# Kernel optimization log

Measured on AMD Instinct MI355X. Metric: run time of the kernel, lower is better.

Reference implementation:

```python
import math
import jax, jax.numpy as jnp
import numpy as np

D = 512
H = 8
HD = D // H
FF = 2048
EPS = 1e-5


def _layernorm(x, gamma, beta):
    mean = jnp.mean(x, axis=-1, keepdims=True)
    var = jnp.mean((x - mean) ** 2, axis=-1, keepdims=True)
    return gamma * (x - mean) / jnp.sqrt(var + EPS) + beta


def _attention(q, k, v, mask):
    # q,k,v: [B,H,Sq/Sk,hd]; mask: [B,Sq,Sk] additive, broadcast over heads
    scale = 1.0 / math.sqrt(q.shape[-1])
    scores = jnp.einsum('bhqd,bhkd->bhqk', q, k) * scale
    scores = scores + mask[:, None, :, :]
    probs = jax.nn.softmax(scores, axis=-1)
    return jnp.einsum('bhqk,bhkd->bhqd', probs, v)


def setup_inputs() -> dict:
    key = jax.random.key(0)
    ks = jax.random.split(key, 20)
    B, S_ENC, S_DEC = 256, 512, 64
    s = 0.02
    inp = {
        'x': jax.random.normal(ks[0], (B, S_ENC, D), jnp.float32),
        'y': jax.random.normal(ks[1], (B, S_DEC, D), jnp.float32),
        'mask': jnp.zeros((B, S_DEC, S_DEC), jnp.float32),
        'mask2': jnp.zeros((B, S_DEC, S_ENC), jnp.float32),
        # self-attention params
        'qkv_w': jax.random.normal(ks[2], (D, 3 * D), jnp.float32) * s,
        'qkv_b': jnp.zeros((3 * D,), jnp.float32),
        'sa_out_w': jax.random.normal(ks[3], (D, D), jnp.float32) * s,
        'sa_out_b': jnp.zeros((D,), jnp.float32),
        # cross-attention params
        'q_w': jax.random.normal(ks[4], (D, D), jnp.float32) * s,
        'q_b': jnp.zeros((D,), jnp.float32),
        'kv_w': jax.random.normal(ks[5], (D, 2 * D), jnp.float32) * s,
        'kv_b': jnp.zeros((2 * D,), jnp.float32),
        'ca_out_w': jax.random.normal(ks[6], (D, D), jnp.float32) * s,
        'ca_out_b': jnp.zeros((D,), jnp.float32),
        # ffn params
        'l1_w': jax.random.normal(ks[7], (D, FF), jnp.float32) * s,
        'l1_b': jnp.zeros((FF,), jnp.float32),
        'l2_w': jax.random.normal(ks[8], (FF, D), jnp.float32) * s,
        'l2_b': jnp.zeros((D,), jnp.float32),
        # layernorm params
        'g1': jnp.ones((D,), jnp.float32), 'b1': jnp.zeros((D,), jnp.float32),
        'g2': jnp.ones((D,), jnp.float32), 'b2': jnp.zeros((D,), jnp.float32),
        'g3': jnp.ones((D,), jnp.float32), 'b3': jnp.zeros((D,), jnp.float32),
    }
    return inp


def reference(x, y, mask, mask2, qkv_w, qkv_b, sa_out_w, sa_out_b,
              q_w, q_b, kv_w, kv_b, ca_out_w, ca_out_b,
              l1_w, l1_b, l2_w, l2_b, g1, b1, g2, b2, g3, b3):
    B, Sd, _ = y.shape
    Se = x.shape[1]

    # --- self attention (post-norm, dropout is identity at eval) ---
    resid = y
    qkv = y @ qkv_w + qkv_b                     # [B,Sd,3D]
    qkv = qkv.reshape(B, Sd, H, 3 * HD).transpose(0, 2, 1, 3)
    q, k, v = jnp.split(qkv, 3, axis=-1)        # each [B,H,Sd,hd]
    vals = _attention(q, k, v, mask)
    vals = vals.transpose(0, 2, 1, 3).reshape(B, Sd, D)
    y = vals @ sa_out_w + sa_out_b
    y = _layernorm(y + resid, g1, b1)

    # --- cross attention: kv from encoder x, q from decoder y ---
    resid = y
    kv = x @ kv_w + kv_b                        # [B,Se,2D]
    kv = kv.reshape(B, Se, H, 2 * HD).transpose(0, 2, 1, 3)
    k, v = jnp.split(kv, 2, axis=-1)            # each [B,H,Se,hd]
    q = (y @ q_w + q_b).reshape(B, Sd, H, HD).transpose(0, 2, 1, 3)
    vals = _attention(q, k, v, mask2)
    vals = vals.transpose(0, 2, 1, 3).reshape(B, Sd, D)
    y = vals @ ca_out_w + ca_out_b
    y = _layernorm(y + resid, g2, b2)

    # --- feed forward ---
    resid = y
    h = jax.nn.relu(y @ l1_w + l1_b)
    y = h @ l2_w + l2_b
    y = _layernorm(y + resid, g3, b3)
    return y
```

## Files before the change

### kernel.cpp

```cpp
#include <hip/hip_runtime.h>
#include <hip/hip_bf16.h>
#include <stdint.h>


#define SDEC 64
#define SENC 512
#define DMODEL 512
#define FFDIM 2048

typedef __bf16 bf16x8 __attribute__((ext_vector_type(8)));
typedef float  f32x4  __attribute__((ext_vector_type(4)));

static __device__ __forceinline__ float bf2f(unsigned short u) {
  union { unsigned int i; float f; } w; w.i = ((unsigned int)u) << 16; return w.f;
}
static __device__ __forceinline__ unsigned short f2bf(float f) {
  union { float f; unsigned int i; } w; w.f = f;
  unsigned int u = w.i;
  return (unsigned short)((u + 0x7fffu + ((u >> 16) & 1u)) >> 16);
}

static __device__ __forceinline__ void gl_lds16(const unsigned short* g, unsigned short* l) {
  __builtin_amdgcn_global_load_lds(
      (const __attribute__((address_space(1))) unsigned int*)g,
      (__attribute__((address_space(3))) unsigned int*)l,
      16, 0, 0);
}

__global__ __launch_bounds__(256)
void cvt_f32_bf16(const float* __restrict__ in, unsigned short* __restrict__ out, size_t n8)
{
  size_t i = (size_t)blockIdx.x * blockDim.x + threadIdx.x;
  const size_t stride = (size_t)gridDim.x * blockDim.x;
  for (; i < n8; i += stride) {
    const float* p = in + i * 8;
    float4 a = *(const float4*)p, b = *(const float4*)(p + 4);
    union { unsigned short s[8]; uint4 v; } u;
    u.s[0] = f2bf(a.x); u.s[1] = f2bf(a.y); u.s[2] = f2bf(a.z); u.s[3] = f2bf(a.w);
    u.s[4] = f2bf(b.x); u.s[5] = f2bf(b.y); u.s[6] = f2bf(b.z); u.s[7] = f2bf(b.w);
    *(uint4*)(out + i * 8) = u.v;
  }
}

#define GEMM_COMPUTE(asrc, bsrc)                                                     \
  {                                                                                  \
    const unsigned short* as_ = (asrc);                                              \
    const unsigned short* bs_ = (bsrc);                                              \
    bf16x8 af[4], bfr[4];                                                            \
    _Pragma("unroll")                                                                \
    for (int mi = 0; mi < 4; ++mi)                                                   \
      af[mi] = *(const bf16x8*)&as_[(wm * 64 + mi * 16 + fr) * 32 + fk];             \
    _Pragma("unroll")                                                                \
    for (int ni = 0; ni < 4; ++ni)                                                   \
      bfr[ni] = *(const bf16x8*)&bs_[(wn * 64 + ni * 16 + fr) * 32 + fk];            \
    _Pragma("unroll")                                                                \
    for (int mi = 0; mi < 4; ++mi)                                                   \
      _Pragma("unroll")                                                              \
      for (int ni = 0; ni < 4; ++ni)                                                 \
        acc[mi][ni] = __builtin_amdgcn_mfma_f32_16x16x32_bf16(af[mi], bfr[ni],       \
                                                              acc[mi][ni], 0, 0, 0); \
  }

template<int RELU>
__global__ __launch_bounds__(256, 2)
void gemm_kernel(const unsigned short* __restrict__ A, const unsigned short* __restrict__ Bt,
                 const float* __restrict__ bias, unsigned short* __restrict__ C,
                 int M, int N, int K)
{
  __shared__ unsigned short sh[2 * 8192];
  const int tid = threadIdx.x;

  const int gx   = gridDim.x;
  const int nwg  = gx * gridDim.y;
  const int orig = blockIdx.y * gx + blockIdx.x;
  const int wg   = (orig & 7) * (nwg >> 3) + (orig >> 3);
  const int row0 = (wg / gx) * 128;
  const int col0 = (wg % gx) * 128;

  const int w = tid >> 6, lane = tid & 63;
  const int wm = w >> 1, wn = w & 1;
  const int gr = lane >> 2, gc = (lane & 3) * 8;

  auto STAGE = [&](int k0, int buf) {
    unsigned short* as = sh + buf * 8192;
    unsigned short* bs = as + 4096;
    #pragma unroll
    for (int i = 0; i < 2; ++i) {
      const int rbase = w * 32 + i * 16;
      gl_lds16(A  + (size_t)(row0 + rbase + gr) * K + (k0 + gc), as + rbase * 32);
      gl_lds16(Bt + (size_t)(col0 + rbase + gr) * K + (k0 + gc), bs + rbase * 32);
    }
  };

  f32x4 acc[4][4];
  #pragma unroll
  for (int i = 0; i < 4; ++i)
    #pragma unroll
    for (int j = 0; j < 4; ++j)
      acc[i][j] = (f32x4){0.f, 0.f, 0.f, 0.f};

  const int fr = lane & 15, fk = (lane >> 4) * 8;

  STAGE(0, 0);
  int cur = 0;
  for (int k0 = 0; k0 + 32 < K; k0 += 32) {
    STAGE(k0 + 32, cur ^ 1);
    asm volatile("s_waitcnt vmcnt(4)" ::: "memory");
    __builtin_amdgcn_s_barrier();
    asm volatile("" ::: "memory");
    GEMM_COMPUTE(sh + cur * 8192, sh + cur * 8192 + 4096);
    asm volatile("" ::: "memory");
    __builtin_amdgcn_s_barrier();
    cur ^= 1;
  }
  asm volatile("s_waitcnt vmcnt(0)" ::: "memory");
  __builtin_amdgcn_s_barrier();
  asm volatile("" ::: "memory");
  GEMM_COMPUTE(sh + cur * 8192, sh + cur * 8192 + 4096);
  asm volatile("" ::: "memory");
  __builtin_amdgcn_s_barrier();

  {
    const int fq = lane >> 4;
    #pragma unroll
    for (int ni = 0; ni < 4; ++ni) {
      const int c = wn * 64 + ni * 16 + fr;
      const float bv = bias ? bias[col0 + c] : 0.f;
      #pragma unroll
      for (int mi = 0; mi < 4; ++mi) {
        #pragma unroll
        for (int t = 0; t < 4; ++t) {
          const int r = wm * 64 + mi * 16 + fq * 4 + t;
          float v = acc[mi][ni][t] + bv;
          if (RELU) v = fmaxf(v, 0.f);
          sh[r * 128 + (c ^ (fq << 4))] = f2bf(v);
        }
      }
    }
    __syncthreads();
    const int rr = tid >> 4;
    const int cc = (tid & 15) * 8;
    #pragma unroll
    for (int p = 0; p < 8; ++p) {
      const int r = p * 16 + rr;
      *(uint4*)(C + (size_t)(row0 + r) * N + col0 + cc) =
          *(const uint4*)&sh[r * 128 + (cc ^ (w << 4))];
    }
  }
}

template<int RELU>
__global__ __launch_bounds__(512, 1)
void gemm256_kernel(const unsigned short* __restrict__ A, const unsigned short* __restrict__ Bt,
                    const float* __restrict__ bias, unsigned short* __restrict__ C,
                    int M, int N, int K)
{
  __shared__ unsigned short sh[65536];
  const int tid = threadIdx.x;

  const int gx   = gridDim.x;
  const int nwg  = gx * gridDim.y;
  const int orig = blockIdx.y * gx + blockIdx.x;
  const int wg   = (orig & 7) * (nwg >> 3) + (orig >> 3);
  const int row0 = (wg / gx) * 256;
  const int col0 = (wg % gx) * 256;

  const int w = tid >> 6, lane = tid & 63;
  const int wm = w >> 2, wn = w & 3;
  const int fr = lane & 15, fg = lane >> 4;

  const int srl = lane >> 3;
  const int sgc = ((lane & 7) ^ srl) * 8;

  auto STAGE_PART = [&](int k0, int buf, int part) {
    unsigned short* base = sh + buf * 32768 + ((part >= 2) ? 16384 : 0);
    const unsigned short* G = (part >= 2) ? Bt : A;
    const int o0 = (part >= 2) ? col0 : row0;
    const int ph = part & 1;
    #pragma unroll
    for (int j = 0; j < 2; ++j) {
      const int rt = w * 32 + ph * 16 + j * 8;
      gl_lds16(G + (size_t)(o0 + rt + srl) * K + (k0 + sgc), base + rt * 64);
    }
  };

  f32x4 acc[8][4];
  #pragma unroll
  for (int i = 0; i < 8; ++i)
    #pragma unroll
    for (int j = 0; j < 4; ++j)
      acc[i][j] = (f32x4){0.f, 0.f, 0.f, 0.f};

  const int NT = K >> 6;
  #pragma unroll
  for (int part = 0; part < 4; ++part) STAGE_PART(0, 0, part);

  for (int t = 0; t < NT; ++t) {
    const int buf = t & 1;
    const unsigned short* as = sh + buf * 32768;
    const unsigned short* bs = as + 16384;
    const int kn = (t + 1) << 6;
    asm volatile("s_waitcnt vmcnt(0)" ::: "memory");
    __builtin_amdgcn_sched_barrier(0);
    __builtin_amdgcn_s_barrier();

    #pragma unroll
    for (int ks = 0; ks < 2; ++ks) {
      #pragma unroll
      for (int mh = 0; mh < 2; ++mh) {
        bf16x8 af[4], bfv[4];
        #pragma unroll
        for (int i = 0; i < 4; ++i) {
          const int row = wm * 128 + (mh * 4 + i) * 16 + fr;
          af[i] = *(const bf16x8*)&as[row * 64 + (((ks * 4 + fg) ^ (fr & 7)) * 8)];
        }
        #pragma unroll
        for (int i = 0; i < 4; ++i) {
          const int row = wn * 64 + i * 16 + fr;
          bfv[i] = *(const bf16x8*)&bs[row * 64 + (((ks * 4 + fg) ^ (fr & 7)) * 8)];
        }
        if (t + 1 < NT) {
          const int ph = ks * 2 + mh;
          if (ph == 0) { STAGE_PART(kn, buf ^ 1, 0); STAGE_PART(kn, buf ^ 1, 1); }
          if (ph == 1) { STAGE_PART(kn, buf ^ 1, 2); STAGE_PART(kn, buf ^ 1, 3); }
        }
        asm volatile("" ::: "memory");
        __builtin_amdgcn_s_barrier();
        __builtin_amdgcn_s_setprio(1);
        #pragma unroll
        for (int i = 0; i < 4; ++i)
          #pragma unroll
          for (int j = 0; j < 4; ++j)
            acc[mh * 4 + i][j] = __builtin_amdgcn_mfma_f32_16x16x32_bf16(
                af[i], bfv[j], acc[mh * 4 + i][j], 0, 0, 0);
        __builtin_amdgcn_s_setprio(0);
        asm volatile("" ::: "memory");
        __builtin_amdgcn_s_barrier();
      }
    }
  }

  {
    #pragma unroll
    for (int j = 0; j < 4; ++j) {
      const int c = wn * 64 + j * 16 + fr;
      const float bv = bias ? bias[col0 + c] : 0.f;
      const int cp = c ^ (fg << 4);
      #pragma unroll
      for (int i = 0; i < 8; ++i) {
        #pragma unroll
        for (int tt = 0; tt < 4; ++tt) {
          const int r = wm * 128 + i * 16 + fg * 4 + tt;
          float v = acc[i][j][tt] + bv;
          if (RELU) v = fmaxf(v, 0.f);
          sh[r * 256 + cp] = f2bf(v);
        }
      }
    }
    __syncthreads();
    const int rr = tid >> 5;
    const int cc = (tid & 31) * 8;
    #pragma unroll
    for (int p = 0; p < 16; ++p) {
      const int r = p * 16 + rr;
      const int rc = (r >> 2) & 3;
      *(uint4*)(C + (size_t)(row0 + r) * N + col0 + cc) =
          *(const uint4*)&sh[r * 256 + (cc ^ (rc << 4))];
    }
  }
}

__global__ __launch_bounds__(256, 2)
void attn_mfma(const unsigned short* __restrict__ qbuf, int qstride, int qmul,
               const unsigned short* __restrict__ kvbuf, int kvstride, int kmul, int kadd,
               int tokmul, int Skv, const float* __restrict__ mask,
               unsigned short* __restrict__ vals, float scale)
{
  __shared__ unsigned short Qs[64 * 72];
  __shared__ unsigned short Ks[64 * 72];
  __shared__ unsigned short Vt[64 * 72];
  __shared__ unsigned short Ps[64 * 72];

  const int nwg  = gridDim.x * gridDim.y;
  const int orig = blockIdx.y * gridDim.x + blockIdx.x;
  const int wg   = (orig & 7) * (nwg >> 3) + (orig >> 3);
  const int h = wg & 7, b = wg >> 3;

  const int tid = threadIdx.x;
  const int w = tid >> 6, lane = tid & 63;
  const int srow = tid >> 2;
  const int sc0 = (tid & 3) * 16;

  {
    const unsigned short* qg = qbuf + (size_t)(b * 64 + srow) * qstride + h * qmul + sc0;
    *(uint4*)&Qs[srow * 72 + sc0]     = *(const uint4*)qg;
    *(uint4*)&Qs[srow * 72 + sc0 + 8] = *(const uint4*)(qg + 8);
  }

  const int fr = lane & 15;
  const int fg = lane >> 4;
  const int orow = fg * 4;

  float mstate[4], lstate[4];
  f32x4 oacc[4];
  #pragma unroll
  for (int t = 0; t < 4; ++t) { mstate[t] = -1e30f; lstate[t] = 0.f; }
  #pragma unroll
  for (int ni = 0; ni < 4; ++ni) oacc[ni] = (f32x4){0.f, 0.f, 0.f, 0.f};

  for (int j0 = 0; j0 < Skv; j0 += 64) {
    __syncthreads();
    {
      const unsigned short* kg = kvbuf + (size_t)(b * tokmul + j0 + srow) * kvstride
                                 + h * kmul + kadd + sc0;
      *(uint4*)&Ks[srow * 72 + sc0]     = *(const uint4*)kg;
      *(uint4*)&Ks[srow * 72 + sc0 + 8] = *(const uint4*)(kg + 8);
      const unsigned short* vg = kg + 64;
      uint4 v0 = *(const uint4*)vg;
      uint4 v1 = *(const uint4*)(vg + 8);
      const unsigned short* vsp = (const unsigned short*)&v0;
      #pragma unroll
      for (int jj = 0; jj < 8; ++jj) Vt[(sc0 + jj) * 72 + srow] = vsp[jj];
      vsp = (const unsigned short*)&v1;
      #pragma unroll
      for (int jj = 0; jj < 8; ++jj) Vt[(sc0 + 8 + jj) * 72 + srow] = vsp[jj];
    }
    __syncthreads();

    f32x4 s[4];
    #pragma unroll
    for (int ni = 0; ni < 4; ++ni) s[ni] = (f32x4){0.f, 0.f, 0.f, 0.f};
    #pragma unroll
    for (int ks = 0; ks < 2; ++ks) {
      bf16x8 aq = *(const bf16x8*)&Qs[(w * 16 + fr) * 72 + ks * 32 + fg * 8];
      #pragma unroll
      for (int ni = 0; ni < 4; ++ni) {
        bf16x8 bk = *(const bf16x8*)&Ks[(ni * 16 + fr) * 72 + ks * 32 + fg * 8];
        s[ni] = __builtin_amdgcn_mfma_f32_16x16x32_bf16(aq, bk, s[ni], 0, 0, 0);
      }
    }

    #pragma unroll
    for (int t = 0; t < 4; ++t) {
      const int grow = w * 16 + orow + t;
      const float* mrow = mask + ((size_t)b * 64 + grow) * Skv + j0;
      float sv[4];
      float tmax = -1e30f;
      #pragma unroll
      for (int ni = 0; ni < 4; ++ni) {
        sv[ni] = s[ni][t] * scale + mrow[ni * 16 + fr];
        tmax = fmaxf(tmax, sv[ni]);
      }
      #pragma unroll
      for (int off = 1; off < 16; off <<= 1) tmax = fmaxf(tmax, __shfl_xor(tmax, off));
      const float mn = fmaxf(mstate[t], tmax);
      const float fscl = __expf(mstate[t] - mn);
      mstate[t] = mn;
      float psum = 0.f;
      #pragma unroll
      for (int ni = 0; ni < 4; ++ni) {
        float p = __expf(sv[ni] - mn);
        psum += p;
        Ps[grow * 72 + ni * 16 + fr] = f2bf(p);
      }
      #pragma unroll
      for (int off = 1; off < 16; off <<= 1) psum += __shfl_xor(psum, off);
      lstate[t] = lstate[t] * fscl + psum;
      #pragma unroll
      for (int ni = 0; ni < 4; ++ni) oacc[ni][t] *= fscl;
    }
    __syncthreads();

    #pragma unroll
    for (int ks = 0; ks < 2; ++ks) {
      bf16x8 pa = *(const bf16x8*)&Ps[(w * 16 + fr) * 72 + ks * 32 + fg * 8];
      #pragma unroll
      for (int ni = 0; ni < 4; ++ni) {
        bf16x8 vb = *(const bf16x8*)&Vt[(ni * 16 + fr) * 72 + ks * 32 + fg * 8];
        oacc[ni] = __builtin_amdgcn_mfma_f32_16x16x32_bf16(pa, vb, oacc[ni], 0, 0, 0);
      }
    }
  }

  #pragma unroll
  for (int t = 0; t < 4; ++t) {
    const int grow = w * 16 + orow + t;
    const float inv = 1.f / lstate[t];
    unsigned short* og = vals + (size_t)(b * 64 + grow) * DMODEL + h * 64;
    #pragma unroll
    for (int ni = 0; ni < 4; ++ni)
      og[ni * 16 + fr] = f2bf(oacc[ni][t] * inv);
  }
}

__global__ __launch_bounds__(256)
void ln_kernel(const unsigned short* __restrict__ proj16, const float* __restrict__ resid32,
               const unsigned short* __restrict__ resid16,
               const float* __restrict__ gamma, const float* __restrict__ beta,
               unsigned short* __restrict__ out16, float* __restrict__ out32)
{
  const int w = threadIdx.x >> 6, lane = threadIdx.x & 63;
  const size_t r = (size_t)blockIdx.x * 4 + w;
  const int d0 = lane * 8;

  float x[8];
  {
    uint4 u = *(const uint4*)(proj16 + r * DMODEL + d0);
    const unsigned short* s = (const unsigned short*)&u;
    #pragma unroll
    for (int j = 0; j < 8; ++j) x[j] = bf2f(s[j]);
  }
  if (resid32) {
    const float* p = resid32 + r * DMODEL + d0;
    float4 a = *(const float4*)p, b = *(const float4*)(p + 4);
    x[0] += a.x; x[1] += a.y; x[2] += a.z; x[3] += a.w;
    x[4] += b.x; x[5] += b.y; x[6] += b.z; x[7] += b.w;
  } else {
    uint4 u = *(const uint4*)(resid16 + r * DMODEL + d0);
    const unsigned short* s = (const unsigned short*)&u;
    #pragma unroll
    for (int j = 0; j < 8; ++j) x[j] += bf2f(s[j]);
  }

  float sum = 0.f;
  #pragma unroll
  for (int j = 0; j < 8; ++j) sum += x[j];
  #pragma unroll
  for (int off = 32; off > 0; off >>= 1) sum += __shfl_xor(sum, off);
  const float mean = sum * (1.f / DMODEL);

  float vs = 0.f;
  #pragma unroll
  for (int j = 0; j < 8; ++j) { float t = x[j] - mean; vs += t * t; }
  #pragma unroll
  for (int off = 32; off > 0; off >>= 1) vs += __shfl_xor(vs, off);
  const float rstd = rsqrtf(vs * (1.f / DMODEL) + 1e-5f);

  float4 g0 = *(const float4*)(gamma + d0), g1 = *(const float4*)(gamma + d0 + 4);
  float4 b0 = *(const float4*)(beta + d0),  b1 = *(const float4*)(beta + d0 + 4);
  const float g[8]  = {g0.x, g0.y, g0.z, g0.w, g1.x, g1.y, g1.z, g1.w};
  const float bb[8] = {b0.x, b0.y, b0.z, b0.w, b1.x, b1.y, b1.z, b1.w};
  float y[8];
  #pragma unroll
  for (int j = 0; j < 8; ++j) y[j] = g[j] * (x[j] - mean) * rstd + bb[j];

  if (out16) {
    union { unsigned short s[8]; uint4 v; } p;
    #pragma unroll
    for (int j = 0; j < 8; ++j) p.s[j] = f2bf(y[j]);
    *(uint4*)(out16 + r * DMODEL + d0) = p.v;
  }
  if (out32) {
    float* o = out32 + r * DMODEL + d0;
    *(float4*)o       = (float4){y[0], y[1], y[2], y[3]};
    *(float4*)(o + 4) = (float4){y[4], y[5], y[6], y[7]};
  }
}

__global__ __launch_bounds__(256)
void transpose_cvt(const float* __restrict__ W, unsigned short* __restrict__ Wt,
                   int K, int N)
{
  __shared__ float tile[32][33];
  const int tx = threadIdx.x, ty = threadIdx.y;
  const int n = blockIdx.x * 32 + tx;
  #pragma unroll
  for (int rr = 0; rr < 4; ++rr) {
    const int k = blockIdx.y * 32 + ty + rr * 8;
    tile[ty + rr * 8][tx] = W[(size_t)k * N + n];
  }
  __syncthreads();
  const int k2 = blockIdx.y * 32 + tx;
  #pragma unroll
  for (int rr = 0; rr < 4; ++rr) {
    const int n2 = blockIdx.x * 32 + ty + rr * 8;
    Wt[(size_t)n2 * K + k2] = f2bf(tile[tx][ty + rr * 8]);
  }
}

extern "C" void kernel_launch(void* const* d_in, const int* in_sizes, int n_in,
                              void* d_out, int out_size, void* d_ws, size_t ws_size,
                              hipStream_t stream)
{
  const float* x        = (const float*)d_in[0];
  const float* y        = (const float*)d_in[1];
  const float* mask     = (const float*)d_in[2];
  const float* mask2    = (const float*)d_in[3];
  const float* qkv_w    = (const float*)d_in[4];
  const float* qkv_b    = (const float*)d_in[5];
  const float* sa_out_w = (const float*)d_in[6];
  const float* sa_out_b = (const float*)d_in[7];
  const float* q_w      = (const float*)d_in[8];
  const float* q_b      = (const float*)d_in[9];
  const float* kv_w     = (const float*)d_in[10];
  const float* kv_b     = (const float*)d_in[11];
  const float* ca_out_w = (const float*)d_in[12];
  const float* ca_out_b = (const float*)d_in[13];
  const float* l1_w     = (const float*)d_in[14];
  const float* l1_b     = (const float*)d_in[15];
  const float* l2_w     = (const float*)d_in[16];
  const float* l2_b     = (const float*)d_in[17];
  const float* g1 = (const float*)d_in[18];
  const float* b1 = (const float*)d_in[19];
  const float* g2 = (const float*)d_in[20];
  const float* b2 = (const float*)d_in[21];
  const float* g3 = (const float*)d_in[22];
  const float* b3 = (const float*)d_in[23];

  const int B  = in_sizes[1] / (SDEC * DMODEL);
  const int M  = B * SDEC;
  const int ME = B * SENC;

  char* ws = (char*)d_ws;
  size_t off = 0;
  auto alloc = [&](size_t bytes) -> char* {
    char* p = ws + off;
    off += (bytes + 255) & ~(size_t)255;
    return p;
  };
  unsigned short* qkv_wt = (unsigned short*)alloc((size_t)1536 * 512 * 2);
  unsigned short* sa_wt  = (unsigned short*)alloc((size_t)512 * 512 * 2);
  unsigned short* q_wt   = (unsigned short*)alloc((size_t)512 * 512 * 2);
  unsigned short* kv_wt  = (unsigned short*)alloc((size_t)1024 * 512 * 2);
  unsigned short* ca_wt  = (unsigned short*)alloc((size_t)512 * 512 * 2);
  unsigned short* l1_wt  = (unsigned short*)alloc((size_t)2048 * 512 * 2);
  unsigned short* l2_wt  = (unsigned short*)alloc((size_t)512 * 2048 * 2);
  unsigned short* kvb    = (unsigned short*)alloc((size_t)ME * 1024 * 2);
  char*           xreg   = alloc((size_t)ME * 512 * 2);
  unsigned short* xb     = (unsigned short*)xreg;
  unsigned short* qkvb   = (unsigned short*)xreg;
  unsigned short* qb     = (unsigned short*)xreg;
  unsigned short* y2b    = (unsigned short*)(xreg + (size_t)16777216);
  unsigned short* valsb  = (unsigned short*)(xreg + (size_t)50331648);
  unsigned short* proj   = (unsigned short*)(xreg + (size_t)67108864);
  unsigned short* y1b    = (unsigned short*)(xreg + (size_t)100663296);
  unsigned short* yb     = (unsigned short*)(xreg + (size_t)117440512);
  unsigned short* hb     = kvb;
  (void)ws_size; (void)n_in; (void)out_size;

  dim3 tb(32, 8);
  transpose_cvt<<<dim3(1536 / 32, 512 / 32), tb, 0, stream>>>(qkv_w, qkv_wt, 512, 1536);
  transpose_cvt<<<dim3(512 / 32, 512 / 32), tb, 0, stream>>>(sa_out_w, sa_wt, 512, 512);
  transpose_cvt<<<dim3(512 / 32, 512 / 32), tb, 0, stream>>>(q_w, q_wt, 512, 512);
  transpose_cvt<<<dim3(1024 / 32, 512 / 32), tb, 0, stream>>>(kv_w, kv_wt, 512, 1024);
  transpose_cvt<<<dim3(512 / 32, 512 / 32), tb, 0, stream>>>(ca_out_w, ca_wt, 512, 512);
  transpose_cvt<<<dim3(2048 / 32, 512 / 32), tb, 0, stream>>>(l1_w, l1_wt, 512, 2048);
  transpose_cvt<<<dim3(512 / 32, 2048 / 32), tb, 0, stream>>>(l2_w, l2_wt, 2048, 512);

  const float scale = 0.125f;

  cvt_f32_bf16<<<4096, 256, 0, stream>>>(x, xb, (size_t)ME * 512 / 8);
  gemm256_kernel<0><<<dim3(1024 / 256, ME / 256), 512, 0, stream>>>(xb, kv_wt, kv_b, kvb, ME, 1024, 512);

  cvt_f32_bf16<<<4096, 256, 0, stream>>>(y, yb, (size_t)M * 512 / 8);
  gemm256_kernel<0><<<dim3(1536 / 256, M / 256), 512, 0, stream>>>(yb, qkv_wt, qkv_b, qkvb, M, 1536, 512);
  attn_mfma<<<dim3(8, B), 256, 0, stream>>>(qkvb, 1536, 192, qkvb, 1536, 192, 64, SDEC, SDEC, mask, valsb, scale);
  gemm_kernel<0><<<dim3(512 / 128, M / 128), 256, 0, stream>>>(valsb, sa_wt, sa_out_b, proj, M, 512, 512);
  ln_kernel<<<M / 4, 256, 0, stream>>>(proj, y, nullptr, g1, b1, y1b, nullptr);

  gemm_kernel<0><<<dim3(512 / 128, M / 128), 256, 0, stream>>>(y1b, q_wt, q_b, qb, M, 512, 512);
  attn_mfma<<<dim3(8, B), 256, 0, stream>>>(qb, 512, 64, kvb, 1024, 128, 0, SENC, SENC, mask2, valsb, scale);
  gemm_kernel<0><<<dim3(512 / 128, M / 128), 256, 0, stream>>>(valsb, ca_wt, ca_out_b, proj, M, 512, 512);
  ln_kernel<<<M / 4, 256, 0, stream>>>(proj, nullptr, y1b, g2, b2, y2b, nullptr);

  gemm256_kernel<1><<<dim3(2048 / 256, M / 256), 512, 0, stream>>>(y2b, l1_wt, l1_b, hb, M, 2048, 512);
  gemm_kernel<0><<<dim3(512 / 128, M / 128), 256, 0, stream>>>(hb, l2_wt, l2_b, proj, M, 512, 2048);
  ln_kernel<<<M / 4, 256, 0, stream>>>(proj, nullptr, y2b, g3, b3, nullptr, (float*)d_out);
}
```

Baseline: 624.1 us.

## Triple-buffer 256-tile GEMM with BK=32 and swizzle 128-tile LDS reads

The 256x256 GEMM moves from a double-buffered K=64 pipeline, which had barriers around every MFMA phase, to a triple-buffered K=32 pipeline. Loads run two tiles ahead with a partial vmcnt wait and one barrier per iteration, cutting LDS use to 96KB. The epilogue writes out in two halves so it fits the smaller shared buffer. Both GEMM kernels also gain an XOR swizzle on the 32-wide LDS rows to cut bank conflicts, at the cost of more loop iterations and a shallower per-tile compute phase.

```diff
diff --git a/kernel.cpp b/kernel.cpp
--- a/kernel.cpp
+++ b/kernel.cpp
@@ -49,10 +49,10 @@
     bf16x8 af[4], bfr[4];                                                            \
     _Pragma("unroll")                                                                \
     for (int mi = 0; mi < 4; ++mi)                                                   \
-      af[mi] = *(const bf16x8*)&as_[(wm * 64 + mi * 16 + fr) * 32 + fk];             \
+      af[mi] = *(const bf16x8*)&as_[(wm * 64 + mi * 16 + fr) * 32 + fsw];            \
     _Pragma("unroll")                                                                \
     for (int ni = 0; ni < 4; ++ni)                                                   \
-      bfr[ni] = *(const bf16x8*)&bs_[(wn * 64 + ni * 16 + fr) * 32 + fk];            \
+      bfr[ni] = *(const bf16x8*)&bs_[(wn * 64 + ni * 16 + fr) * 32 + fsw];           \
     _Pragma("unroll")                                                                \
     for (int mi = 0; mi < 4; ++mi)                                                   \
       _Pragma("unroll")                                                              \
@@ -79,7 +79,8 @@
 
   const int w = tid >> 6, lane = tid & 63;
   const int wm = w >> 1, wn = w & 1;
-  const int gr = lane >> 2, gc = (lane & 3) * 8;
+  const int gr = lane >> 2;
+  const int gc = ((lane & 3) ^ ((lane >> 3) & 3)) * 8;
 
   auto STAGE = [&](int k0, int buf) {
     unsigned short* as = sh + buf * 8192;
@@ -99,7 +100,9 @@
     for (int j = 0; j < 4; ++j)
       acc[i][j] = (f32x4){0.f, 0.f, 0.f, 0.f};
 
-  const int fr = lane & 15, fk = (lane >> 4) * 8;
+  const int fr  = lane & 15;
+  const int fg  = lane >> 4;
+  const int fsw = (fg ^ ((fr >> 1) & 3)) * 8;
 
   STAGE(0, 0);
   int cur = 0;
@@ -155,7 +158,7 @@
                     const float* __restrict__ bias, unsigned short* __restrict__ C,
                     int M, int N, int K)
 {
-  __shared__ unsigned short sh[65536];
+  __shared__ unsigned short sh[3 * 16384];
   const int tid = threadIdx.x;
 
   const int gx   = gridDim.x;
@@ -167,21 +170,19 @@
 
   const int w = tid >> 6, lane = tid & 63;
   const int wm = w >> 2, wn = w & 3;
-  const int fr = lane & 15, fg = lane >> 4;
-
-  const int srl = lane >> 3;
-  const int sgc = ((lane & 7) ^ srl) * 8;
-
-  auto STAGE_PART = [&](int k0, int buf, int part) {
-    unsigned short* base = sh + buf * 32768 + ((part >= 2) ? 16384 : 0);
+  const int fr  = lane & 15;
+  const int fg  = lane >> 4;
+  const int fsw = (fg ^ ((fr >> 1) & 3)) * 8;
+
+  const int gr = lane >> 2;
+  const int gc = ((lane & 3) ^ ((lane >> 3) & 3)) * 8;
+
+  auto STAGE = [&](int t, int buf, int part) {
+    unsigned short* base = sh + buf * 16384 + ((part >= 2) ? 8192 : 0);
     const unsigned short* G = (part >= 2) ? Bt : A;
     const int o0 = (part >= 2) ? col0 : row0;
-    const int ph = part & 1;
-    #pragma unroll
-    for (int j = 0; j < 2; ++j) {
-      const int rt = w * 32 + ph * 16 + j * 8;
-      gl_lds16(G + (size_t)(o0 + rt + srl) * K + (k0 + sgc), base + rt * 64);
-    }
+    const int rbase = (part & 1) * 128 + w * 16;
+    gl_lds16(G + (size_t)(o0 + rbase + gr) * K + (t * 32 + gc), base + rbase * 32);
   };
 
   f32x4 acc[8][4];
@@ -191,69 +192,68 @@
     for (int j = 0; j < 4; ++j)
       acc[i][j] = (f32x4){0.f, 0.f, 0.f, 0.f};
 
-  const int NT = K >> 6;
-  #pragma unroll
-  for (int part = 0; part < 4; ++part) STAGE_PART(0, 0, part);
-
+  const int NT = K >> 5;
+  #pragma unroll
+  for (int part = 0; part < 4; ++part) STAGE(0, 0, part);
+  #pragma unroll
+  for (int part = 0; part < 4; ++part) STAGE(1, 1, part);
+
+  int bc = 0, bp = 2;
   for (int t = 0; t < NT; ++t) {
-    const int buf = t & 1;
-    const unsigned short* as = sh + buf * 32768;
-    const unsigned short* bs = as + 16384;
-    const int kn = (t + 1) << 6;
-    asm volatile("s_waitcnt vmcnt(0)" ::: "memory");
+    if (t == NT - 1) asm volatile("s_waitcnt vmcnt(0)" ::: "memory");
+    else             asm volatile("s_waitcnt vmcnt(4)" ::: "memory");
     __builtin_amdgcn_sched_barrier(0);
     __builtin_amdgcn_s_barrier();
-
-    #pragma unroll
-    for (int ks = 0; ks < 2; ++ks) {
-      #pragma unroll
-      for (int mh = 0; mh < 2; ++mh) {
-        bf16x8 af[4], bfv[4];
+    asm volatile("" ::: "memory");
+
+    const unsigned short* as = sh + bc * 16384;
+    const unsigned short* bs = as + 8192;
+    bf16x8 bfv[4];
+    #pragma unroll
+    for (int j = 0; j < 4; ++j)
+      bfv[j] = *(const bf16x8*)&bs[(wn * 64 + j * 16 + fr) * 32 + fsw];
+
+    #pragma unroll
+    for (int mh = 0; mh < 2; ++mh) {
+      if (t + 2 < NT) {
+        STAGE(t + 2, bp, mh * 2);
+        STAGE(t + 2, bp, mh * 2 + 1);
+      }
+      bf16x8 af[4];
+      #pragma unroll
+      for (int i = 0; i < 4; ++i)
+        af[i] = *(const bf16x8*)&as[(wm * 128 + (mh * 4 + i) * 16 + fr) * 32 + fsw];
+      __builtin_amdgcn_s_setprio(1);
+      #pragma unroll
+      for (int i = 0; i < 4; ++i)
         #pragma unroll
-        for (int i = 0; i < 4; ++i) {
-          const int row = wm * 128 + (mh * 4 + i) * 16 + fr;
-          af[i] = *(const bf16x8*)&as[row * 64 + (((ks * 4 + fg) ^ (fr & 7)) * 8)];
-        }
+        for (int j = 0; j < 4; ++j)
+          acc[mh * 4 + i][j] = __builtin_amdgcn_mfma_f32_16x16x32_bf16(
+              af[i], bfv[j], acc[mh * 4 + i][j], 0, 0, 0);
+      __builtin_amdgcn_s_setprio(0);
+    }
+    bc = (bc + 1 == 3) ? 0 : bc + 1;
+    bp = (bp + 1 == 3) ? 0 : bp + 1;
+  }
+
+  #pragma unroll
+  for (int p = 0; p < 2; ++p) {
+    __syncthreads();
+    if (wm == p) {
+      #pragma unroll
+      for (int j = 0; j < 4; ++j) {
+        const int c = wn * 64 + j * 16 + fr;
+        const float bv = bias ? bias[col0 + c] : 0.f;
+        const int cp = c ^ (fg << 4);
         #pragma unroll
-        for (int i = 0; i < 4; ++i) {
-          const int row = wn * 64 + i * 16 + fr;
-          bfv[i] = *(const bf16x8*)&bs[row * 64 + (((ks * 4 + fg) ^ (fr & 7)) * 8)];
-        }
-        if (t + 1 < NT) {
-          const int ph = ks * 2 + mh;
-          if (ph == 0) { STAGE_PART(kn, buf ^ 1, 0); STAGE_PART(kn, buf ^ 1, 1); }
-          if (ph == 1) { STAGE_PART(kn, buf ^ 1, 2); STAGE_PART(kn, buf ^ 1, 3); }
-        }
-        asm volatile("" ::: "memory");
-        __builtin_amdgcn_s_barrier();
-        __builtin_amdgcn_s_setprio(1);
-        #pragma unroll
-        for (int i = 0; i < 4; ++i)
+        for (int i = 0; i < 8; ++i) {
           #pragma unroll
-          for (int j = 0; j < 4; ++j)
-            acc[mh * 4 + i][j] = __builtin_amdgcn_mfma_f32_16x16x32_bf16(
-                af[i], bfv[j], acc[mh * 4 + i][j], 0, 0, 0);
-        __builtin_amdgcn_s_setprio(0);
-        asm volatile("" ::: "memory");
-        __builtin_amdgcn_s_barrier();
-      }
-    }
-  }
-
-  {
-    #pragma unroll
-    for (int j = 0; j < 4; ++j) {
-      const int c = wn * 64 + j * 16 + fr;
-      const float bv = bias ? bias[col0 + c] : 0.f;
-      const int cp = c ^ (fg << 4);
-      #pragma unroll
-      for (int i = 0; i < 8; ++i) {
-        #pragma unroll
-        for (int tt = 0; tt < 4; ++tt) {
-          const int r = wm * 128 + i * 16 + fg * 4 + tt;
-          float v = acc[i][j][tt] + bv;
-          if (RELU) v = fmaxf(v, 0.f);
-          sh[r * 256 + cp] = f2bf(v);
+          for (int tt = 0; tt < 4; ++tt) {
+            const int r = i * 16 + fg * 4 + tt;
+            float v = acc[i][j][tt] + bv;
+            if (RELU) v = fmaxf(v, 0.f);
+            sh[r * 256 + cp] = f2bf(v);
+          }
         }
       }
     }
@@ -261,10 +261,10 @@
     const int rr = tid >> 5;
     const int cc = (tid & 31) * 8;
     #pragma unroll
-    for (int p = 0; p < 16; ++p) {
-      const int r = p * 16 + rr;
+    for (int q = 0; q < 8; ++q) {
+      const int r = q * 16 + rr;
       const int rc = (r >> 2) & 3;
-      *(uint4*)(C + (size_t)(row0 + r) * N + col0 + cc) =
+      *(uint4*)(C + (size_t)(row0 + p * 128 + r) * N + col0 + cc) =
           *(const uint4*)&sh[r * 256 + (cc ^ (rc << 4))];
     }
   }
```

Measured after the change: 632.9 us. About the same (+1.4%).
